# Kernel tuning notes

Hardware: AMD Instinct MI355X
Metric: run time of the kernel (lower is better)

Reference implementation:

```python
import jax, jax.numpy as jnp
import numpy as np
from jax import lax

NQ = 5  # qubits
NL = 3  # circuit layers


def conv2d(x, w, b):
    y = lax.conv_general_dilated(x, w, (1, 1), 'SAME',
                                 dimension_numbers=('NCHW', 'OIHW', 'NCHW'))
    return y + b[None, :, None, None]


def batchnorm(x, g, b, eps=1e-5):
    # training-mode batch statistics over (N,H,W), matching nn.BatchNorm2d in train()
    mu = x.mean((0, 2, 3), keepdims=True)
    var = x.var((0, 2, 3), keepdims=True)
    return g[None, :, None, None] * (x - mu) * lax.rsqrt(var + eps) + b[None, :, None, None]


def maxpool2(x):
    return lax.reduce_window(x, -jnp.inf, lax.max, (1, 1, 2, 2), (1, 1, 2, 2), 'VALID')


def _apply_1q(state, U, w):
    # state: (2,)*NQ, wire w is axis w (PennyLane default.qubit ordering)
    s = jnp.tensordot(U, state, axes=([1], [w]))
    return jnp.moveaxis(s, 0, w)


def _cnot(state, c, t):
    s0 = jnp.take(state, 0, axis=c)
    s1 = jnp.take(state, 1, axis=c)
    ta = t if t < c else t - 1
    s1 = jnp.flip(s1, axis=ta)  # X on target when control=1
    return jnp.stack([s0, s1], axis=c)


def _rx(t):
    c, s = jnp.cos(t / 2), jnp.sin(t / 2)
    return jnp.array([[c, -1j * s], [-1j * s, c]], dtype=jnp.complex64)


def _ry(t):
    c, s = jnp.cos(t / 2), jnp.sin(t / 2)
    return jnp.array([[c, -s], [s, c]], dtype=jnp.complex64)


def _rz(t):
    e = jnp.exp(-1j * t / 2)
    z = jnp.zeros((), jnp.complex64)
    return jnp.array([[e, z], [z, jnp.conj(e)]], dtype=jnp.complex64)


def quantum_circuit(inputs, weights):
    # inputs: (5,), weights: (30,)  -> scalar <Z0 Z1 Z2>
    state = jnp.zeros((2,) * NQ, jnp.complex64).at[(0,) * NQ].set(1.0)
    npl = NQ * 2  # weights per layer = 10
    nw = weights.shape[0]
    for l in range(NL):
        for i in range(NQ):
            state = _apply_1q(state, _rx(inputs[i]), i)
        for i in range(NQ):
            state = _apply_1q(state, _ry(weights[(l * npl + i) % nw]), i)
            state = _apply_1q(state, _rz(weights[(l * npl + i + NQ) % nw]), i)
        for i in range(NQ - 1):
            state = _cnot(state, i, i + 1)
        state = _cnot(state, NQ - 1, 0)
    probs = jnp.abs(state) ** 2
    z = jnp.array([1.0, -1.0], jnp.float32)
    sign = z[:, None, None] * z[None, :, None] * z[None, None, :]  # Z on wires 0,1,2
    return jnp.sum(probs * sign[:, :, :, None, None])


def setup_inputs() -> dict:
    key = jax.random.key(0)
    ks = jax.random.split(key, 12)
    d = {}
    d['x'] = jax.random.normal(ks[0], (256, 1, 224, 224), jnp.float32)
    d['conv1_w'] = jax.random.normal(ks[1], (16, 1, 3, 3), jnp.float32) * 0.1
    d['conv1_b'] = jnp.zeros((16,), jnp.float32)
    d['bn1_g'] = jnp.ones((16,), jnp.float32)
    d['bn1_b'] = jnp.zeros((16,), jnp.float32)
    d['conv2_w'] = jax.random.normal(ks[2], (32, 16, 3, 3), jnp.float32) * 0.05
    d['conv2_b'] = jnp.zeros((32,), jnp.float32)
    d['bn2_g'] = jnp.ones((32,), jnp.float32)
    d['bn2_b'] = jnp.zeros((32,), jnp.float32)
    d['conv3_w'] = jax.random.normal(ks[3], (64, 32, 3, 3), jnp.float32) * 0.05
    d['conv3_b'] = jnp.zeros((64,), jnp.float32)
    d['bn3_g'] = jnp.ones((64,), jnp.float32)
    d['bn3_b'] = jnp.zeros((64,), jnp.float32)
    d['fc1_w'] = jax.random.normal(ks[4], (64, 5), jnp.float32) * 0.1   # (in,out)
    d['fc1_b'] = jnp.zeros((5,), jnp.float32)
    d['ln_g'] = jnp.ones((5,), jnp.float32)
    d['ln_b'] = jnp.zeros((5,), jnp.float32)
    d['q_params'] = jax.random.uniform(ks[5], (30,), jnp.float32)
    d['fc2_w'] = jax.random.normal(ks[6], (1, 32), jnp.float32) * 0.5
    d['fc2_b'] = jnp.zeros((32,), jnp.float32)
    d['fc3_w'] = jax.random.normal(ks[7], (32, 2), jnp.float32) * 0.2
    d['fc3_b'] = jnp.zeros((2,), jnp.float32)
    return d


def reference(x, conv1_w, conv1_b, bn1_g, bn1_b, conv2_w, conv2_b, bn2_g, bn2_b,
              conv3_w, conv3_b, bn3_g, bn3_b, fc1_w, fc1_b, ln_g, ln_b,
              q_params, fc2_w, fc2_b, fc3_w, fc3_b):
    h = maxpool2(jax.nn.relu(batchnorm(conv2d(x, conv1_w, conv1_b), bn1_g, bn1_b)))
    h = maxpool2(jax.nn.relu(batchnorm(conv2d(h, conv2_w, conv2_b), bn2_g, bn2_b)))
    h = maxpool2(jax.nn.relu(batchnorm(conv2d(h, conv3_w, conv3_b), bn3_g, bn3_b)))
    # dropout is identity in eval; adaptive avg pool (1,1) + flatten
    h = h.mean((2, 3))                    # (B, 64)
    h = h @ fc1_w + fc1_b                 # (B, 5)
    mu = h.mean(-1, keepdims=True)
    var = h.var(-1, keepdims=True)
    h = ln_g * (h - mu) * lax.rsqrt(var + 1e-5) + ln_b
    q = jax.vmap(lambda inp: quantum_circuit(inp, q_params))(h)  # (B,)
    q = q[:, None].astype(jnp.float32)    # (B, 1)
    h2 = jax.nn.relu(q @ fc2_w + fc2_b)   # (B, 32)
    logits = h2 @ fc3_w + fc3_b           # (B, 2)
    return jax.nn.log_softmax(logits, axis=1)
```

## Files before the change

### kernel.cpp

```cpp
#include <hip/hip_runtime.h>
#include <hip/hip_bf16.h>


typedef _Float16 f16;
typedef _Float16 f16x2 __attribute__((ext_vector_type(2)));
typedef _Float16 f16x4 __attribute__((ext_vector_type(4)));
typedef _Float16 f16x8 __attribute__((ext_vector_type(8)));
typedef float f32x4 __attribute__((ext_vector_type(4)));
typedef float f32x16 __attribute__((ext_vector_type(16)));

#define DEV static __device__ __forceinline__

DEV float wave_sum(float v) {
#pragma unroll
  for (int off = 32; off > 0; off >>= 1) v += __shfl_xor(v, off, 64);
  return v;
}

__global__ __launch_bounds__(256) void repack(const float* __restrict__ w2,
                                              const float* __restrict__ w3,
                                              f16* __restrict__ Bt2,
                                              f16* __restrict__ Bt3) {
  int t = blockIdx.x * 256 + threadIdx.x;
  int T = gridDim.x * 256;
  for (int i = t; i < 32 * 168; i += T) {
    int oc = i / 168, kk = i - oc * 168;
    float v = 0.f;
    if (kk < 144) {
      int tap = kk >> 4, ic = kk & 15;
      v = w2[(oc * 16 + ic) * 9 + tap];
    }
    Bt2[i] = (f16)v;
  }
  for (int i = t; i < 64 * 296; i += T) {
    int oc = i / 296, kk = i - oc * 296;
    float v = 0.f;
    if (kk < 288) {
      int tap = kk / 32, ic = kk & 31;
      v = w3[(oc * 32 + ic) * 9 + tap];
    }
    Bt3[i] = (f16)v;
  }
}

__global__ __launch_bounds__(64) void finalize(const float* __restrict__ banks,
                                               const float* __restrict__ g,
                                               const float* __restrict__ b,
                                               float* __restrict__ scsh, int C,
                                               float inv_n) {
  int c = blockIdx.x, bk = threadIdx.x;
  float s = banks[bk * 2 * C + c];
  float qq = banks[bk * 2 * C + C + c];
  s = wave_sum(s);
  qq = wave_sum(qq);
  if (bk == 0) {
    float mean = s * inv_n;
    float var = qq * inv_n - mean * mean;
    float sc = g[c] * rsqrtf(var + 1e-5f);
    scsh[c] = sc;
    scsh[C + c] = b[c] - mean * sc;
  }
}

__global__ __launch_bounds__(256) void l1_mfma32(const float* __restrict__ x,
                                                 const float* __restrict__ w1,
                                                 float* __restrict__ banks,
                                                 f16* __restrict__ h1raw) {
  __shared__ f16 xA[18 * 240];
  __shared__ f16 xB[18 * 240];
  __shared__ f16 lrow[4 * 3616];
  __shared__ float lstat[32];
  int bid = blockIdx.x;
  int n = bid / 14, band = bid - n * 14;
  int y0 = band * 16;
  int t = threadIdx.x;
  if (t < 32) lstat[t] = 0.f;
  for (int i = t; i < 1008; i += 256) {
    int r = i / 56, k = i - r * 56;
    int y = y0 - 1 + r;
    float4 v = make_float4(0.f, 0.f, 0.f, 0.f);
    if ((unsigned)y < 224u)
      v = *(const float4*)(x + ((size_t)(n * 224 + y)) * 224 + k * 4);
    f16 h0 = (f16)v.x, h1 = (f16)v.y, h2 = (f16)v.z, h3 = (f16)v.w;
    f16* pa = xA + r * 240 + 4 * k + 1;
    pa[0] = h0; pa[1] = h1; pa[2] = h2; pa[3] = h3;
    f16x4 pk = {h0, h1, h2, h3};
    *(f16x4*)(xB + r * 240 + 4 * k) = pk;
  }
  if (t < 18) {
    xA[t * 240 + 0] = (f16)0.f;
    xA[t * 240 + 225] = (f16)0.f;
    xA[t * 240 + 226] = (f16)0.f;
    xB[t * 240 + 224] = (f16)0.f;
    xB[t * 240 + 225] = (f16)0.f;
  }
  __syncthreads();

  int wave = t >> 6, lane = t & 63;
  int g = lane >> 5, m32 = lane & 31;
  int oc = m32 & 15, s = m32 >> 4;

  f16x8 b;
#pragma unroll
  for (int j = 0; j < 8; j++) {
    int ky = 2 * g + (j >> 2), kx = j & 3;
    int kys = ky - s;
    float wv = 0.f;
    if (kx < 3 && kys >= 0 && kys < 3) wv = w1[oc * 9 + kys * 3 + kx];
    b[j] = (f16)wv;
  }

  const f16* abase = (m32 & 1) ? (xB + (m32 - 1)) : (xA + m32);
  f16* myrow = lrow + wave * 3616;
  f16* mrow = myrow + s * 1808;
  f32x16 zero16;
#pragma unroll
  for (int r = 0; r < 16; r++) zero16[r] = 0.f;
  const int bp[8] = {0, 1, 4, 5, 8, 9, 12, 13};
  float ssum = 0.f, ssq = 0.f;

  for (int rp = wave; rp < 8; rp += 4) {
    int r0 = 2 * rp + 2 * g;
    const f16* rbase = abase + r0 * 240;
#pragma unroll
    for (int xt = 0; xt < 7; xt++) {
      const f16* p0 = rbase + xt * 32;
      f16x2 v0 = *(const f16x2*)(p0);
      f16x2 v1 = *(const f16x2*)(p0 + 2);
      f16x2 v2 = *(const f16x2*)(p0 + 240);
      f16x2 v3 = *(const f16x2*)(p0 + 242);
      f16x8 a = {v0[0], v0[1], v1[0], v1[1], v2[0], v2[1], v3[0], v3[1]};
      f32x16 acc = __builtin_amdgcn_mfma_f32_32x32x16_f16(a, b, zero16, 0, 0, 0);
#pragma unroll
      for (int r = 0; r < 16; r++) {
        float v = acc[r];
        ssum += v;
        ssq += v * v;
      }
#pragma unroll
      for (int i = 0; i < 8; i++) {
        float pm = fmaxf(acc[2 * i], acc[2 * i + 1]);
        int pxp = xt * 16 + bp[i] + 2 * g;
        mrow[pxp * 16 + oc] = (f16)pm;
      }
    }
    int ph = band * 8 + rp;
    f16* gdst = h1raw + ((size_t)(n * 112) + ph) * 112 * 16;
    for (int i = lane; i < 224; i += 64) {
      f16x8 va = *(const f16x8*)(myrow + i * 8);
      f16x8 vb = *(const f16x8*)(myrow + 1808 + i * 8);
#pragma unroll
      for (int k = 0; k < 8; k++) va[k] = (va[k] > vb[k]) ? va[k] : vb[k];
      *(f16x8*)(gdst + i * 8) = va;
    }
  }
  ssum += __shfl_xor(ssum, 16, 64);
  ssum += __shfl_xor(ssum, 32, 64);
  ssq += __shfl_xor(ssq, 16, 64);
  ssq += __shfl_xor(ssq, 32, 64);
  if (lane < 16) {
    atomicAdd(&lstat[oc], ssum);
    atomicAdd(&lstat[16 + oc], ssq);
  }
  __syncthreads();
  if (t < 32) atomicAdd(&banks[(bid & 63) * 32 + t], lstat[t]);
}

__global__ __launch_bounds__(256) void l2_gemm(const f16* __restrict__ h1,
                                               const f16* __restrict__ Btg,
                                               const float* __restrict__ scsh1,
                                               f16* __restrict__ p2,
                                               float* __restrict__ banks) {
  extern __shared__ char smem[];
  f16* lin = (f16*)smem;
  f16* lB = (f16*)(smem + 21888);
  f16* lpool = (f16*)(smem + 32640);
  float* lstat = (float*)(smem + 39808);
  int bid = blockIdx.x;
  int n = bid / 28, band = bid - n * 28, h0 = band * 4;
  int t = threadIdx.x;
  if (t < 64) lstat[t] = 0.f;
  {
    const uint4* s = (const uint4*)Btg;
    uint4* d = (uint4*)lB;
    for (int i = t; i < 672; i += 256) d[i] = s[i];
  }
  {
    for (int i = t; i < 1344; i += 256) {
      int r = i / 224, c = i - r * 224;
      int y = h0 + r - 1;
      f16x8 o = {0, 0, 0, 0, 0, 0, 0, 0};
      if ((unsigned)y < 112u) {
        f16x8 xv =
            *(const f16x8*)(h1 + ((size_t)(n * 112 + y)) * 112 * 16 + c * 8);
        int ch0 = (c & 1) * 8;
#pragma unroll
        for (int k = 0; k < 8; k++) {
          float f = (float)xv[k] * scsh1[ch0 + k] + scsh1[16 + ch0 + k];
          o[k] = (f16)fmaxf(f, 0.f);
        }
      }
      *(f16x8*)(lin + ((size_t)r * 228 + 2 + c) * 8) = o;
    }
    if (t < 24) {
      int r = t >> 2, k = t & 3;
      f16x8 z = {0, 0, 0, 0, 0, 0, 0, 0};
      *(f16x8*)(lin + ((size_t)r * 228 + ((k < 2) ? k : (226 + k - 2))) * 8) = z;
    }
  }
  __syncthreads();
  int wave = t >> 6, lane = t & 63, q = lane >> 4, wi = lane & 15;
  const int icq = (q & 1) * 8;
  f32x4 acc[7][2];
#pragma unroll
  for (int f = 0; f < 7; f++)
#pragma unroll
    for (int nf = 0; nf < 2; nf++)
#pragma unroll
      for (int r = 0; r < 4; r++) acc[f][nf][r] = 0.f;

#pragma unroll
  for (int j = 0; j < 5; j++) {
    const int tA = 2 * j, tB = 2 * j + 1;
    const int kyA = tA / 3, kxA = tA % 3;
    const int kyB = (tB < 9) ? tB / 3 : 0, kxB = (tB < 9) ? tB % 3 : 0;
    bool hiq = (q >= 2);
    int ky = hiq ? kyB : kyA;
    int kx = hiq ? kxB : kxA;
    const f16* aptr0 = lin + ((wave + ky) * 114 + wi + kx) * 16 + icq;
    bool zq = (j == 4) && hiq;
    const f16* zptr = lB + 152;
    f16x8 b0 = *(const f16x8*)(lB + wi * 168 + j * 32 + q * 8);
    f16x8 b1 = *(const f16x8*)(lB + (16 + wi) * 168 + j * 32 + q * 8);
#pragma unroll
    for (int f = 0; f < 7; f++) {
      const f16* ap = zq ? zptr : (aptr0 + f * 256);
      f16x8 a = *(const f16x8*)ap;
      acc[f][0] = __builtin_amdgcn_mfma_f32_16x16x32_f16(a, b0, acc[f][0], 0, 0, 0);
      acc[f][1] = __builtin_amdgcn_mfma_f32_16x16x32_f16(a, b1, acc[f][1], 0, 0, 0);
    }
  }
  float s0 = 0.f, q0 = 0.f, s1 = 0.f, q1 = 0.f;
#pragma unroll
  for (int f = 0; f < 7; f++)
#pragma unroll
    for (int r = 0; r < 4; r++) {
      float v0 = acc[f][0][r], v1 = acc[f][1][r];
      s0 += v0; q0 += v0 * v0;
      s1 += v1; q1 += v1 * v1;
    }
  s0 += __shfl_xor(s0, 16, 64); s0 += __shfl_xor(s0, 32, 64);
  q0 += __shfl_xor(q0, 16, 64); q0 += __shfl_xor(q0, 32, 64);
  s1 += __shfl_xor(s1, 16, 64); s1 += __shfl_xor(s1, 32, 64);
  q1 += __shfl_xor(q1, 16, 64); q1 += __shfl_xor(q1, 32, 64);
  if (q == 0) {
    atomicAdd(&lstat[wi], s0);
    atomicAdd(&lstat[16 + wi], s1);
    atomicAdd(&lstat[32 + wi], q0);
    atomicAdd(&lstat[48 + wi], q1);
  }
  if (wave & 1) {
#pragma unroll
    for (int f = 0; f < 7; f++)
#pragma unroll
      for (int nf = 0; nf < 2; nf++) {
        int ch = nf * 16 + wi;
        int pc0 = f * 8 + q * 2;
        float m0 = fmaxf(acc[f][nf][0], acc[f][nf][1]);
        float m1 = fmaxf(acc[f][nf][2], acc[f][nf][3]);
        lpool[((wave >> 1) * 56 + pc0) * 32 + ch] = (f16)m0;
        lpool[((wave >> 1) * 56 + pc0 + 1) * 32 + ch] = (f16)m1;
      }
  }
  __syncthreads();
  if (!(wave & 1)) {
    int ph = band * 2 + (wave >> 1);
#pragma unroll
    for (int f = 0; f < 7; f++)
#pragma unroll
      for (int nf = 0; nf < 2; nf++) {
        int ch = nf * 16 + wi;
        int pc0 = f * 8 + q * 2;
        float m0 = fmaxf(acc[f][nf][0], acc[f][nf][1]);
        float m1 = fmaxf(acc[f][nf][2], acc[f][nf][3]);
        m0 = fmaxf(m0, (float)lpool[((wave >> 1) * 56 + pc0) * 32 + ch]);
        m1 = fmaxf(m1, (float)lpool[((wave >> 1) * 56 + pc0 + 1) * 32 + ch]);
        size_t ob = (((size_t)n * 56 + ph) * 56) * 32;
        p2[ob + (size_t)pc0 * 32 + ch] = (f16)m0;
        p2[ob + (size_t)(pc0 + 1) * 32 + ch] = (f16)m1;
      }
  }
  if (t < 64) {
    int i = t >> 5, c = t & 31;
    atomicAdd(&banks[(bid & 63) * 64 + i * 32 + c], lstat[i * 32 + c]);
  }
}

__global__ __launch_bounds__(256) void l3_gemm(const f16* __restrict__ p2,
                                               const f16* __restrict__ Btg,
                                               const float* __restrict__ scsh2,
                                               f16* __restrict__ p3,
                                               float* __restrict__ banks) {
  extern __shared__ char smem[];
  f16* lin = (f16*)smem;
  f16* lB = (f16*)(smem + 22272);
  f16* lpool = (f16*)(smem + 41216);
  float* lstat = (float*)(smem + 48384);
  int bx = blockIdx.x, zo = blockIdx.y;
  int n = bx / 14, band = bx - n * 14, h0 = band * 4;
  int t = threadIdx.x;
  if (t < 64) lstat[t] = 0.f;
  {
    const uint4* s = (const uint4*)(Btg + (size_t)zo * 32 * 296);
    uint4* d = (uint4*)lB;
    for (int i = t; i < 1184; i += 256) d[i] = s[i];
  }
  {
    for (int i = t; i < 1344; i += 256) {
      int r = i / 224, rem = i - r * 224;
      int c = rem >> 2, cp = rem & 3;
      int y = h0 + r - 1;
      f16x8 o = {0, 0, 0, 0, 0, 0, 0, 0};
      if ((unsigned)y < 56u) {
        const f16* src = p2 + (((size_t)(n * 56 + y)) * 56 + c) * 32 + cp * 8;
        f16x8 xv = *(const f16x8*)src;
        int ch0 = cp * 8;
#pragma unroll
        for (int k = 0; k < 8; k++) {
          float f = (float)xv[k] * scsh2[ch0 + k] + scsh2[32 + ch0 + k];
          o[k] = (f16)fmaxf(f, 0.f);
        }
      }
      *(f16x8*)(lin + ((size_t)r * 58 + 1 + c) * 32 + cp * 8) = o;
    }
    if (t < 48) {
      int r = t / 8, k = t & 7;
      int col = (k < 4) ? 0 : 57, cp = k & 3;
      f16x8 z = {0, 0, 0, 0, 0, 0, 0, 0};
      *(f16x8*)(lin + ((size_t)r * 58 + col) * 32 + cp * 8) = z;
    }
  }
  __syncthreads();
  int wave = t >> 6, lane = t & 63, q = lane >> 4, wi = lane & 15;
  int mhalf = wave & 1, nf = wave >> 1;
  int abase[7];
#pragma unroll
  for (int f = 0; f < 7; f++) {
    int pos = mhalf * 112 + f * 16 + wi;
    int r = pos / 56, w = pos - r * 56;
    abase[f] = (r * 58 + w) * 32 + q * 8;
  }
  f32x4 acc[7];
#pragma unroll
  for (int f = 0; f < 7; f++)
#pragma unroll
    for (int r = 0; r < 4; r++) acc[f][r] = 0.f;

#pragma unroll
  for (int j = 0; j < 9; j++) {
    const int ky = j / 3, kx = j % 3;
    f16x8 b = *(const f16x8*)(lB + (nf * 16 + wi) * 296 + j * 32 + q * 8);
#pragma unroll
    for (int f = 0; f < 7; f++) {
      f16x8 a = *(const f16x8*)(lin + abase[f] + (ky * 58 + kx) * 32);
      acc[f] = __builtin_amdgcn_mfma_f32_16x16x32_f16(a, b, acc[f], 0, 0, 0);
    }
  }
  int ch_local = nf * 16 + wi;
  float s0 = 0.f, q0 = 0.f;
#pragma unroll
  for (int f = 0; f < 7; f++)
#pragma unroll
    for (int r = 0; r < 4; r++) {
      float v = acc[f][r];
      s0 += v; q0 += v * v;
    }
  s0 += __shfl_xor(s0, 16, 64); s0 += __shfl_xor(s0, 32, 64);
  q0 += __shfl_xor(q0, 16, 64); q0 += __shfl_xor(q0, 32, 64);
  if (q == 0) {
    atomicAdd(&lstat[ch_local], s0);
    atomicAdd(&lstat[32 + ch_local], q0);
  }
#pragma unroll
  for (int f = 0; f < 7; f++) {
    int pos = mhalf * 112 + f * 16 + q * 4;
    int r0 = pos / 56, w0 = pos - r0 * 56;
    int p2i = pos + 2;
    int r1 = p2i / 56, w1 = p2i - r1 * 56;
    float m0 = fmaxf(acc[f][0], acc[f][1]);
    float m1 = fmaxf(acc[f][2], acc[f][3]);
    lpool[(r0 * 28 + (w0 >> 1)) * 32 + ch_local] = (f16)m0;
    lpool[(r1 * 28 + (w1 >> 1)) * 32 + ch_local] = (f16)m1;
  }
  __syncthreads();
  for (int i = t; i < 1792; i += 256) {
    int ch = i & 31, rest = i >> 5;
    int pc = rest % 28, pr = rest / 28;
    float v = fmaxf((float)lpool[((2 * pr) * 28 + pc) * 32 + ch],
                    (float)lpool[((2 * pr + 1) * 28 + pc) * 32 + ch]);
    int gpr = band * 2 + pr;
    p3[(((size_t)n * 28 + gpr) * 28 + pc) * 64 + zo * 32 + ch] = (f16)v;
  }
  if (t < 64) {
    int i = t >> 5, c = t & 31;
    int bank = (bx * 2 + zo) & 63;
    atomicAdd(&banks[bank * 128 + i * 64 + zo * 32 + c], lstat[i * 32 + c]);
  }
}

__global__ __launch_bounds__(256) void head_pool(
    const f16* __restrict__ p3, const float* __restrict__ scsh3,
    const float* __restrict__ fc1w, const float* __restrict__ fc1b,
    float* __restrict__ featg) {
  int n = blockIdx.x, t = threadIdx.x;
  __shared__ float red[64 * 33];
  __shared__ float meanc[64];
  int oct = t & 7, strip = t >> 3;
  float sc[8], sh[8];
#pragma unroll
  for (int k = 0; k < 8; k++) {
    sc[k] = scsh3[oct * 8 + k];
    sh[k] = scsh3[64 + oct * 8 + k];
  }
  float acc[8];
#pragma unroll
  for (int k = 0; k < 8; k++) acc[k] = 0.f;
  const f16* base = p3 + (size_t)n * 50176 + oct * 8;
  for (int px = strip; px < 784; px += 32) {
    f16x8 v = *(const f16x8*)(base + (size_t)px * 64);
#pragma unroll
    for (int k = 0; k < 8; k++)
      acc[k] += fmaxf((float)v[k] * sc[k] + sh[k], 0.f);
  }
#pragma unroll
  for (int k = 0; k < 8; k++) red[(oct * 8 + k) * 33 + strip] = acc[k];
  __syncthreads();
  if (t < 64) {
    float s = 0.f;
    for (int j = 0; j < 32; j++) s += red[t * 33 + j];
    meanc[t] = s * (1.f / 784.f);
  }
  __syncthreads();
  if (t < 5) {
    float a = fc1b[t];
    for (int i = 0; i < 64; i++) a += meanc[i] * fc1w[i * 5 + t];
    featg[n * 8 + t] = a;
  }
}

template <int W>
DEV void g_rx(float (&sr)[32], float (&si)[32], float c, float s) {
  constexpr int m = 1 << (4 - W);
#pragma unroll
  for (int i0 = 0; i0 < 32; i0++)
    if (!(i0 & m)) {
      int i1 = i0 | m;
      float a0r = sr[i0], a0i = si[i0], a1r = sr[i1], a1i = si[i1];
      sr[i0] = c * a0r + s * a1i;
      si[i0] = c * a0i - s * a1r;
      sr[i1] = s * a0i + c * a1r;
      si[i1] = -s * a0r + c * a1i;
    }
}

template <int W>
DEV void g_ry(float (&sr)[32], float (&si)[32], float c, float s) {
  constexpr int m = 1 << (4 - W);
#pragma unroll
  for (int i0 = 0; i0 < 32; i0++)
    if (!(i0 & m)) {
      int i1 = i0 | m;
      float a0r = sr[i0], a0i = si[i0], a1r = sr[i1], a1i = si[i1];
      sr[i0] = c * a0r - s * a1r;
      si[i0] = c * a0i - s * a1i;
      sr[i1] = s * a0r + c * a1r;
      si[i1] = s * a0i + c * a1i;
    }
}

template <int W>
DEV void g_rz(float (&sr)[32], float (&si)[32], float c, float s) {
  constexpr int m = 1 << (4 - W);
#pragma unroll
  for (int i0 = 0; i0 < 32; i0++)
    if (!(i0 & m)) {
      int i1 = i0 | m;
      float a0r = sr[i0], a0i = si[i0], a1r = sr[i1], a1i = si[i1];
      sr[i0] = c * a0r + s * a0i;
      si[i0] = c * a0i - s * a0r;
      sr[i1] = c * a1r - s * a1i;
      si[i1] = c * a1i + s * a1r;
    }
}

template <int C, int T>
DEV void g_cnot(float (&sr)[32], float (&si)[32]) {
  constexpr int mc = 1 << (4 - C), mt = 1 << (4 - T);
#pragma unroll
  for (int i0 = 0; i0 < 32; i0++)
    if ((i0 & mc) && !(i0 & mt)) {
      int i1 = i0 | mt;
      float tr = sr[i0]; sr[i0] = sr[i1]; sr[i1] = tr;
      float ti = si[i0]; si[i0] = si[i1]; si[i1] = ti;
    }
}

__global__ __launch_bounds__(64) void head_q(
    const float* __restrict__ featg, const float* __restrict__ lng,
    const float* __restrict__ lnb, const float* __restrict__ qp,
    const float* __restrict__ fc2w, const float* __restrict__ fc2b,
    const float* __restrict__ fc3w, const float* __restrict__ fc3b,
    float* __restrict__ out) {
  int n = blockIdx.x * 64 + threadIdx.x;
  float f[5];
#pragma unroll
  for (int i = 0; i < 5; i++) f[i] = featg[n * 8 + i];
  float mu = (f[0] + f[1] + f[2] + f[3] + f[4]) * 0.2f;
  float var = 0.f;
#pragma unroll
  for (int i = 0; i < 5; i++) { float d = f[i] - mu; var += d * d; }
  var *= 0.2f;
  float inv = rsqrtf(var + 1e-5f);
#pragma unroll
  for (int i = 0; i < 5; i++) f[i] = lng[i] * (f[i] - mu) * inv + lnb[i];

  float cx[5], sx[5];
#pragma unroll
  for (int i = 0; i < 5; i++) {
    cx[i] = cosf(0.5f * f[i]);
    sx[i] = sinf(0.5f * f[i]);
  }
  float sr[32], si[32];
#pragma unroll
  for (int i = 0; i < 32; i++) { sr[i] = 0.f; si[i] = 0.f; }
  sr[0] = 1.f;

  for (int l = 0; l < 3; l++) {
    g_rx<0>(sr, si, cx[0], sx[0]);
    g_rx<1>(sr, si, cx[1], sx[1]);
    g_rx<2>(sr, si, cx[2], sx[2]);
    g_rx<3>(sr, si, cx[3], sx[3]);
    g_rx<4>(sr, si, cx[4], sx[4]);
#define WIRE_YZ(I)                                             \
  {                                                            \
    float ty = qp[l * 10 + I];                                 \
    g_ry<I>(sr, si, cosf(0.5f * ty), sinf(0.5f * ty));         \
    float tz = qp[l * 10 + I + 5];                             \
    g_rz<I>(sr, si, cosf(0.5f * tz), sinf(0.5f * tz));         \
  }
    WIRE_YZ(0) WIRE_YZ(1) WIRE_YZ(2) WIRE_YZ(3) WIRE_YZ(4)
#undef WIRE_YZ
    g_cnot<0, 1>(sr, si);
    g_cnot<1, 2>(sr, si);
    g_cnot<2, 3>(sr, si);
    g_cnot<3, 4>(sr, si);
    g_cnot<4, 0>(sr, si);
  }
  float qv = 0.f;
#pragma unroll
  for (int idx = 0; idx < 32; idx++) {
    float p = sr[idx] * sr[idx] + si[idx] * si[idx];
    qv += (__popc(idx & 0x1C) & 1) ? -p : p;
  }
  float l0 = fc3b[0], l1 = fc3b[1];
  for (int j = 0; j < 32; j++) {
    float hv = fmaxf(qv * fc2w[j] + fc2b[j], 0.f);
    l0 += hv * fc3w[j * 2];
    l1 += hv * fc3w[j * 2 + 1];
  }
  float mx = fmaxf(l0, l1);
  float lse = mx + logf(expf(l0 - mx) + expf(l1 - mx));
  out[n * 2 + 0] = l0 - lse;
  out[n * 2 + 1] = l1 - lse;
}

extern "C" void kernel_launch(void* const* d_in, const int* in_sizes, int n_in,
                              void* d_out, int out_size, void* d_ws,
                              size_t ws_size, hipStream_t stream) {
  const float* x    = (const float*)d_in[0];
  const float* w1   = (const float*)d_in[1];
  const float* bn1g = (const float*)d_in[3];
  const float* bn1b = (const float*)d_in[4];
  const float* w2   = (const float*)d_in[5];
  const float* bn2g = (const float*)d_in[7];
  const float* bn2b = (const float*)d_in[8];
  const float* w3   = (const float*)d_in[9];
  const float* bn3g = (const float*)d_in[11];
  const float* bn3b = (const float*)d_in[12];
  const float* fc1w = (const float*)d_in[13];
  const float* fc1b = (const float*)d_in[14];
  const float* lng  = (const float*)d_in[15];
  const float* lnb  = (const float*)d_in[16];
  const float* qp   = (const float*)d_in[17];
  const float* fc2w = (const float*)d_in[18];
  const float* fc2b = (const float*)d_in[19];
  const float* fc3w = (const float*)d_in[20];
  const float* fc3b = (const float*)d_in[21];
  float* out = (float*)d_out;

  char* ws = (char*)d_ws;
  float* banks1 = (float*)ws;
  float* banks2 = (float*)(ws + 8192);
  float* banks3 = (float*)(ws + 24576);
  float* scsh1 = (float*)(ws + 57344);
  float* scsh2 = (float*)(ws + 57472);
  float* scsh3 = (float*)(ws + 57728);
  f16* Bt2 = (f16*)(ws + 58240);
  f16* Bt3 = (f16*)(ws + 68992);
  f16* h1 = (f16*)(ws + 106880);
  f16* p2 = (f16*)(ws + 106880 + 102760448ULL);
  f16* p3 = (f16*)(ws + 106880 + 102760448ULL + 51380224ULL);
  float* featg = banks2;

  hipMemsetAsync(ws, 0, 57344, stream);
  repack<<<16, 256, 0, stream>>>(w2, w3, Bt2, Bt3);
  l1_mfma32<<<3584, 256, 0, stream>>>(x, w1, banks1, h1);
  finalize<<<16, 64, 0, stream>>>(banks1, bn1g, bn1b, scsh1, 16,
                                  1.f / 12845056.f);
  l2_gemm<<<7168, 256, 40064, stream>>>(h1, Bt2, scsh1, p2, banks2);
  finalize<<<32, 64, 0, stream>>>(banks2, bn2g, bn2b, scsh2, 32,
                                  1.f / 3211264.f);
  l3_gemm<<<dim3(3584, 2), 256, 48640, stream>>>(p2, Bt3, scsh2, p3, banks3);
  finalize<<<64, 64, 0, stream>>>(banks3, bn3g, bn3b, scsh3, 64,
                                  1.f / 802816.f);
  head_pool<<<256, 256, 0, stream>>>(p3, scsh3, fc1w, fc1b, featg);
  head_q<<<4, 64, 0, stream>>>(featg, lng, lnb, qp, fc2w, fc2b, fc3w, fc3b,
                               out);
}
```

Measured before the change: 369.6 us.

## Pad LDS input rows against bank conflicts and merge l3 output-channel halves per block

The l2 and l3 input tiles in shared memory get padded per-pixel strides (20 and 36 halves instead of 16 and 32) to reduce LDS bank conflicts on the MFMA A-operand reads. l3_gemm no longer splits the 64 output channels across two grid-y blocks. Each block now computes all 64 channels with two accumulator sets per wave, so the input tile is staged and BN/ReLU-transformed once instead of twice. The trade is more LDS per block (about 78KB), which lowers occupancy, and more accumulator registers.

Result: slower. 537.5 us (+45.4%).

```diff
diff --git a/kernel.cpp b/kernel.cpp
--- a/kernel.cpp
+++ b/kernel.cpp
@@ -173,9 +173,9 @@
                                                float* __restrict__ banks) {
   extern __shared__ char smem[];
   f16* lin = (f16*)smem;
-  f16* lB = (f16*)(smem + 21888);
-  f16* lpool = (f16*)(smem + 32640);
-  float* lstat = (float*)(smem + 39808);
+  f16* lB = (f16*)(smem + 27360);
+  f16* lpool = (f16*)(smem + 38112);
+  float* lstat = (float*)(smem + 45280);
   int bid = blockIdx.x;
   int n = bid / 28, band = bid - n * 28, h0 = band * 4;
   int t = threadIdx.x;
@@ -200,12 +200,14 @@
           o[k] = (f16)fmaxf(f, 0.f);
         }
       }
-      *(f16x8*)(lin + ((size_t)r * 228 + 2 + c) * 8) = o;
+      *(f16x8*)(lin + (r * 114 + 1 + (c >> 1)) * 20 + (c & 1) * 8) = o;
     }
     if (t < 24) {
       int r = t >> 2, k = t & 3;
       f16x8 z = {0, 0, 0, 0, 0, 0, 0, 0};
-      *(f16x8*)(lin + ((size_t)r * 228 + ((k < 2) ? k : (226 + k - 2))) * 8) = z;
+      int addr = (k < 2) ? ((r * 114 + 0) * 20 + k * 8)
+                         : ((r * 114 + 113) * 20 + (k - 2) * 8);
+      *(f16x8*)(lin + addr) = z;
     }
   }
   __syncthreads();
@@ -227,14 +229,14 @@
     bool hiq = (q >= 2);
     int ky = hiq ? kyB : kyA;
     int kx = hiq ? kxB : kxA;
-    const f16* aptr0 = lin + ((wave + ky) * 114 + wi + kx) * 16 + icq;
+    const f16* aptr0 = lin + ((wave + ky) * 114 + wi + kx) * 20 + icq;
     bool zq = (j == 4) && hiq;
     const f16* zptr = lB + 152;
     f16x8 b0 = *(const f16x8*)(lB + wi * 168 + j * 32 + q * 8);
     f16x8 b1 = *(const f16x8*)(lB + (16 + wi) * 168 + j * 32 + q * 8);
 #pragma unroll
     for (int f = 0; f < 7; f++) {
-      const f16* ap = zq ? zptr : (aptr0 + f * 256);
+      const f16* ap = zq ? zptr : (aptr0 + f * 320);
       f16x8 a = *(const f16x8*)ap;
       acc[f][0] = __builtin_amdgcn_mfma_f32_16x16x32_f16(a, b0, acc[f][0], 0, 0, 0);
       acc[f][1] = __builtin_amdgcn_mfma_f32_16x16x32_f16(a, b1, acc[f][1], 0, 0, 0);
@@ -303,17 +305,17 @@
                                                float* __restrict__ banks) {
   extern __shared__ char smem[];
   f16* lin = (f16*)smem;
-  f16* lB = (f16*)(smem + 22272);
-  f16* lpool = (f16*)(smem + 41216);
-  float* lstat = (float*)(smem + 48384);
-  int bx = blockIdx.x, zo = blockIdx.y;
+  f16* lB = (f16*)(smem + 25056);
+  f16* lpool = (f16*)(smem + 62944);
+  float* lstat = (float*)(smem + 77280);
+  int bx = blockIdx.x;
   int n = bx / 14, band = bx - n * 14, h0 = band * 4;
   int t = threadIdx.x;
-  if (t < 64) lstat[t] = 0.f;
+  if (t < 128) lstat[t] = 0.f;
   {
-    const uint4* s = (const uint4*)(Btg + (size_t)zo * 32 * 296);
+    const uint4* s = (const uint4*)Btg;
     uint4* d = (uint4*)lB;
-    for (int i = t; i < 1184; i += 256) d[i] = s[i];
+    for (int i = t; i < 2368; i += 256) d[i] = s[i];
   }
   {
     for (int i = t; i < 1344; i += 256) {
@@ -331,80 +333,90 @@
           o[k] = (f16)fmaxf(f, 0.f);
         }
       }
-      *(f16x8*)(lin + ((size_t)r * 58 + 1 + c) * 32 + cp * 8) = o;
+      *(f16x8*)(lin + (r * 58 + 1 + c) * 36 + cp * 8) = o;
     }
     if (t < 48) {
       int r = t / 8, k = t & 7;
       int col = (k < 4) ? 0 : 57, cp = k & 3;
       f16x8 z = {0, 0, 0, 0, 0, 0, 0, 0};
-      *(f16x8*)(lin + ((size_t)r * 58 + col) * 32 + cp * 8) = z;
+      *(f16x8*)(lin + (r * 58 + col) * 36 + cp * 8) = z;
     }
   }
   __syncthreads();
   int wave = t >> 6, lane = t & 63, q = lane >> 4, wi = lane & 15;
-  int mhalf = wave & 1, nf = wave >> 1;
+  int mhalf = wave & 1, nfpair = wave >> 1;
   int abase[7];
 #pragma unroll
   for (int f = 0; f < 7; f++) {
     int pos = mhalf * 112 + f * 16 + wi;
     int r = pos / 56, w = pos - r * 56;
-    abase[f] = (r * 58 + w) * 32 + q * 8;
-  }
-  f32x4 acc[7];
+    abase[f] = (r * 58 + w) * 36 + q * 8;
+  }
+  f32x4 acc[7][2];
 #pragma unroll
   for (int f = 0; f < 7; f++)
 #pragma unroll
-    for (int r = 0; r < 4; r++) acc[f][r] = 0.f;
+    for (int nf = 0; nf < 2; nf++)
+#pragma unroll
+      for (int r = 0; r < 4; r++) acc[f][nf][r] = 0.f;
 
 #pragma unroll
   for (int j = 0; j < 9; j++) {
     const int ky = j / 3, kx = j % 3;
-    f16x8 b = *(const f16x8*)(lB + (nf * 16 + wi) * 296 + j * 32 + q * 8);
+    f16x8 b0 = *(const f16x8*)(lB + (nfpair * 32 + wi) * 296 + j * 32 + q * 8);
+    f16x8 b1 =
+        *(const f16x8*)(lB + (nfpair * 32 + 16 + wi) * 296 + j * 32 + q * 8);
 #pragma unroll
     for (int f = 0; f < 7; f++) {
-      f16x8 a = *(const f16x8*)(lin + abase[f] + (ky * 58 + kx) * 32);
-      acc[f] = __builtin_amdgcn_mfma_f32_16x16x32_f16(a, b, acc[f], 0, 0, 0);
-    }
-  }
-  int ch_local = nf * 16 + wi;
-  float s0 = 0.f, q0 = 0.f;
+      f16x8 a = *(const f16x8*)(lin + abase[f] + (ky * 58 + kx) * 36);
+      acc[f][0] = __builtin_amdgcn_mfma_f32_16x16x32_f16(a, b0, acc[f][0], 0, 0, 0);
+      acc[f][1] = __builtin_amdgcn_mfma_f32_16x16x32_f16(a, b1, acc[f][1], 0, 0, 0);
+    }
+  }
+  int ch0 = nfpair * 32 + wi, ch1 = ch0 + 16;
+  float s0 = 0.f, q0 = 0.f, s1 = 0.f, q1 = 0.f;
 #pragma unroll
   for (int f = 0; f < 7; f++)
 #pragma unroll
     for (int r = 0; r < 4; r++) {
-      float v = acc[f][r];
-      s0 += v; q0 += v * v;
+      float v0 = acc[f][0][r], v1 = acc[f][1][r];
+      s0 += v0; q0 += v0 * v0;
+      s1 += v1; q1 += v1 * v1;
     }
   s0 += __shfl_xor(s0, 16, 64); s0 += __shfl_xor(s0, 32, 64);
   q0 += __shfl_xor(q0, 16, 64); q0 += __shfl_xor(q0, 32, 64);
+  s1 += __shfl_xor(s1, 16, 64); s1 += __shfl_xor(s1, 32, 64);
+  q1 += __shfl_xor(q1, 16, 64); q1 += __shfl_xor(q1, 32, 64);
   if (q == 0) {
-    atomicAdd(&lstat[ch_local], s0);
-    atomicAdd(&lstat[32 + ch_local], q0);
+    atomicAdd(&lstat[ch0], s0);
+    atomicAdd(&lstat[ch1], s1);
+    atomicAdd(&lstat[64 + ch0], q0);
+    atomicAdd(&lstat[64 + ch1], q1);
   }
 #pragma unroll
   for (int f = 0; f < 7; f++) {
     int pos = mhalf * 112 + f * 16 + q * 4;
     int r0 = pos / 56, w0 = pos - r0 * 56;
-    int p2i = pos + 2;
-    int r1 = p2i / 56, w1 = p2i - r1 * 56;
-    float m0 = fmaxf(acc[f][0], acc[f][1]);
-    float m1 = fmaxf(acc[f][2], acc[f][3]);
-    lpool[(r0 * 28 + (w0 >> 1)) * 32 + ch_local] = (f16)m0;
-    lpool[(r1 * 28 + (w1 >> 1)) * 32 + ch_local] = (f16)m1;
-  }
-  __syncthreads();
-  for (int i = t; i < 1792; i += 256) {
-    int ch = i & 31, rest = i >> 5;
+#pragma unroll
+    for (int nf = 0; nf < 2; nf++) {
+      int ch = nf ? ch1 : ch0;
+      float m0 = fmaxf(acc[f][nf][0], acc[f][nf][1]);
+      float m1 = fmaxf(acc[f][nf][2], acc[f][nf][3]);
+      lpool[(r0 * 28 + (w0 >> 1)) * 64 + ch] = (f16)m0;
+      lpool[(r0 * 28 + (w0 >> 1) + 1) * 64 + ch] = (f16)m1;
+    }
+  }
+  __syncthreads();
+  for (int i = t; i < 3584; i += 256) {
+    int ch = i & 63, rest = i >> 6;
     int pc = rest % 28, pr = rest / 28;
-    float v = fmaxf((float)lpool[((2 * pr) * 28 + pc) * 32 + ch],
-                    (float)lpool[((2 * pr + 1) * 28 + pc) * 32 + ch]);
+    float v = fmaxf((float)lpool[((2 * pr) * 28 + pc) * 64 + ch],
+                    (float)lpool[((2 * pr + 1) * 28 + pc) * 64 + ch]);
     int gpr = band * 2 + pr;
-    p3[(((size_t)n * 28 + gpr) * 28 + pc) * 64 + zo * 32 + ch] = (f16)v;
-  }
-  if (t < 64) {
-    int i = t >> 5, c = t & 31;
-    int bank = (bx * 2 + zo) & 63;
-    atomicAdd(&banks[bank * 128 + i * 64 + zo * 32 + c], lstat[i * 32 + c]);
+    p3[(((size_t)n * 28 + gpr) * 28 + pc) * 64 + ch] = (f16)v;
+  }
+  if (t < 128) {
+    atomicAdd(&banks[(bx & 63) * 128 + t], lstat[t]);
   }
 }
 
@@ -617,10 +629,10 @@
   l1_mfma32<<<3584, 256, 0, stream>>>(x, w1, banks1, h1);
   finalize<<<16, 64, 0, stream>>>(banks1, bn1g, bn1b, scsh1, 16,
                                   1.f / 12845056.f);
-  l2_gemm<<<7168, 256, 40064, stream>>>(h1, Bt2, scsh1, p2, banks2);
+  l2_gemm<<<7168, 256, 45536, stream>>>(h1, Bt2, scsh1, p2, banks2);
   finalize<<<32, 64, 0, stream>>>(banks2, bn2g, bn2b, scsh2, 32,
                                   1.f / 3211264.f);
-  l3_gemm<<<dim3(3584, 2), 256, 48640, stream>>>(p2, Bt3, scsh2, p3, banks3);
+  l3_gemm<<<3584, 256, 77792, stream>>>(p2, Bt3, scsh2, p3, banks3);
   finalize<<<64, 64, 0, stream>>>(banks3, bn3g, bn3b, scsh3, 64,
                                   1.f / 802816.f);
   head_pool<<<256, 256, 0, stream>>>(p3, scsh3, fc1w, fc1b, featg);
```
